# Kernel tuning notes

Hardware: AMD Instinct MI355X
Metric: run time of the kernel (lower is better)

Reference implementation:

```python
import jax, jax.numpy as jnp
import numpy as np

MARGIN = 5.0
VAR_FLOOR = 1e-4
BIG = 1e6


def setup_inputs() -> dict:
    key = jax.random.key(0)
    ks = jax.random.split(key, 8)
    B, D, R = 512, 768, 128
    C_new, C_old = 10, 100
    return {
        "features": jax.random.normal(ks[0], (B, D), jnp.float32),
        "labels": jax.random.randint(ks[1], (B,), 0, C_new),
        "new_class_ids": jnp.arange(C_new),
        "cur_means": jax.random.normal(ks[2], (C_new, D), jnp.float32),
        "cur_bases": jax.random.normal(ks[3], (C_new, D, R), jnp.float32),
        "cur_variances": jax.random.uniform(ks[4], (C_new, R + 1), jnp.float32),
        "calibrated_old_means": jax.random.normal(ks[5], (C_old, D), jnp.float32),
        "calibrated_old_bases": jax.random.normal(ks[6], (C_old, D, R), jnp.float32),
        "calibrated_old_variances": jax.random.uniform(ks[7], (C_old, R + 1), jnp.float32),
    }


def _geometry_distance_matrix(z, means, bases, variances):
    # z: [B,D], means: [C,D], bases: [C,D,R], variances: [C,R+1] -> [B,C]
    diff = z[:, None, :] - means[None, :, :]                    # [B,C,D]
    coeff = jnp.einsum('bcd,cdr->bcr', diff, bases)             # [B,C,R]
    eig = jnp.maximum(variances[:, :-1], VAR_FLOOR)             # [C,R]
    res = jnp.maximum(variances[:, -1], VAR_FLOOR)              # [C]
    parallel = jnp.sum(coeff * coeff / eig[None, :, :], axis=-1)  # [B,C]
    recon = jnp.einsum('bcr,cdr->bcd', coeff, bases)            # [B,C,D]
    residual_term = jnp.sum((diff - recon) ** 2, axis=-1) / res[None, :]
    dist = (parallel + residual_term) / z.shape[1]              # normalize_by_dim
    return jnp.nan_to_num(dist, nan=BIG, posinf=BIG, neginf=BIG)


def reference(features, labels, new_class_ids, cur_means, cur_bases, cur_variances,
              calibrated_old_means, calibrated_old_bases, calibrated_old_variances):
    z = jnp.nan_to_num(features, nan=0.0, posinf=0.0, neginf=0.0)  # [B,D]
    labels = labels.reshape(-1)

    own_all = _geometry_distance_matrix(z, cur_means, cur_bases, cur_variances)  # [B,C_new_total]
    old_all = _geometry_distance_matrix(z, calibrated_old_means, calibrated_old_bases,
                                        calibrated_old_variances)               # [B,C_old]
    old_min = jnp.min(old_all, axis=1)                                           # [B]

    # Per-new-class masks; union of class masks reproduces new_mask implicitly.
    masks = (labels[None, :] == new_class_ids[:, None]).astype(z.dtype)          # [K,B]
    counts = masks.sum(axis=1)                                                   # [K]
    denom = jnp.maximum(counts, 1.0)

    own_k = own_all[:, new_class_ids].T                                          # [K,B]
    hinge = jax.nn.relu(MARGIN + own_k - old_min[None, :])                       # [K,B]

    total_k = (hinge * masks).sum(axis=1) / denom
    own_k_mean = (own_k * masks).sum(axis=1) / denom
    old_k_mean = (old_min[None, :] * masks).sum(axis=1) / denom

    valid = (counts > 0).astype(z.dtype)
    n_valid = jnp.maximum(valid.sum(), 1.0)
    total = (total_k * valid).sum() / n_valid
    own = (own_k_mean * valid).sum() / n_valid
    old = (old_k_mean * valid).sum() / n_valid
    return jnp.stack([total, own, old])  # [total, own, old]
```

## Files before the change

### kernel.cpp

```cpp
#include <hip/hip_runtime.h>
#include <hip/hip_bf16.h>
#include <math.h>
#include <stdint.h>

#define B_N   512
#define D_N   768
#define R_N   128
#define C_NEW 10
#define C_OLD 100
#define C_TOT 110
#define MARGIN_F    5.0f
#define VAR_FLOOR_F 1e-4f
#define BIG_F       1e6f

typedef __bf16 bf16;
typedef __bf16 bf16x4 __attribute__((ext_vector_type(4)));
typedef __bf16 bf16x8 __attribute__((ext_vector_type(8)));
typedef float  f32x4  __attribute__((ext_vector_type(4)));

__device__ __forceinline__ float cleanf(float v) { return isfinite(v) ? v : 0.0f; }

__device__ __forceinline__ unsigned encf(float f) {
    unsigned u = __float_as_uint(f);
    return (u & 0x80000000u) ? ~u : (u | 0x80000000u);
}
__device__ __forceinline__ float decf(unsigned u) {
    return (u & 0x80000000u) ? __uint_as_float(u & 0x7fffffffu) : __uint_as_float(~u);
}

__global__ __launch_bounds__(256)
void prep_fused(const float* __restrict__ z,
                const float* __restrict__ cur_means, const float* __restrict__ old_means,
                const float* __restrict__ cur_bases, const float* __restrict__ old_bases,
                bf16* __restrict__ zbf, float* __restrict__ znorm, float* __restrict__ munorm,
                bf16* __restrict__ basesT, unsigned* __restrict__ ominE)
{
    const int bid = blockIdx.x;
    const int tid = threadIdx.x, wave = tid >> 6, lane = tid & 63;
    __shared__ bf16 T[128][128];
    __shared__ float s4[4];

    if (bid < 128) {
        const int b = bid * 4 + wave;
        const float4* src = (const float4*)(z + (size_t)b * D_N);
        bf16x4* dst = (bf16x4*)(zbf + (size_t)b * D_N);
        float nrm = 0.f;
        #pragma unroll
        for (int i = 0; i < 3; ++i) {
            float4 v = src[lane + i * 64];
            v.x = cleanf(v.x); v.y = cleanf(v.y); v.z = cleanf(v.z); v.w = cleanf(v.w);
            nrm += v.x * v.x + v.y * v.y + v.z * v.z + v.w * v.w;
            bf16x4 w;
            w[0] = (bf16)v.x; w[1] = (bf16)v.y; w[2] = (bf16)v.z; w[3] = (bf16)v.w;
            dst[lane + i * 64] = w;
        }
        #pragma unroll
        for (int off = 32; off >= 1; off >>= 1) nrm += __shfl_xor(nrm, off, 64);
        if (lane == 0) { znorm[b] = nrm; ominE[b] = 0xFFFFFFFFu; }
        return;
    }

    if (bid < 128 + C_TOT) {
        const int c = bid - 128;
        const float* mu = (c < C_NEW) ? cur_means + (size_t)c * D_N
                                      : old_means + (size_t)(c - C_NEW) * D_N;
        float p = 0.f;
        for (int d = tid; d < D_N; d += 256) p += mu[d] * mu[d];
        #pragma unroll
        for (int off = 32; off >= 1; off >>= 1) p += __shfl_xor(p, off, 64);
        if (lane == 0) s4[wave] = p;
        __syncthreads();
        if (tid == 0) munorm[c] = s4[0] + s4[1] + s4[2] + s4[3];
        return;
    }

    const int tb = bid - (128 + C_TOT);
    const int dt = tb % 6, c = tb / 6;
    const float* Bc = (c < C_NEW) ? cur_bases + (size_t)c * D_N * R_N
                                  : old_bases + (size_t)(c - C_NEW) * D_N * R_N;
    const int d0 = dt * 128;
    const int rg  = tid & 31;
    const int dgb = tid >> 5;

    #pragma unroll
    for (int i = 0; i < 4; ++i) {
        const int dg = i * 8 + dgb;
        const float* src = Bc + (size_t)(d0 + dg * 4) * R_N + rg * 4;
        float4 v0 = *(const float4*)(src);
        float4 v1 = *(const float4*)(src + R_N);
        float4 v2 = *(const float4*)(src + 2 * R_N);
        float4 v3 = *(const float4*)(src + 3 * R_N);
        const float* f0 = (const float*)&v0;
        const float* f1 = (const float*)&v1;
        const float* f2 = (const float*)&v2;
        const float* f3 = (const float*)&v3;
        #pragma unroll
        for (int j = 0; j < 4; ++j) {
            const int R = rg * 4 + j;
            const int pc = dg ^ (R & 31);
            bf16x4 w;
            w[0] = (bf16)f0[j]; w[1] = (bf16)f1[j]; w[2] = (bf16)f2[j]; w[3] = (bf16)f3[j];
            *(bf16x4*)(&T[R][pc * 4]) = w;
        }
    }
    __syncthreads();

    #pragma unroll
    for (int it = 0; it < 16; ++it) {
        const int q = it * 256 + tid;
        const int r = q >> 5, u = q & 31;
        const int pc = u ^ (r & 31);
        ushort4 w = *(const ushort4*)(&T[r][pc * 4]);
        *(ushort4*)(basesT + (size_t)c * R_N * D_N + (size_t)r * D_N + d0 + u * 4) = w;
    }
}

__global__ __launch_bounds__(256)
void gram(const bf16* __restrict__ basesT,
          const float* __restrict__ cur_means, const float* __restrict__ old_means,
          bf16* __restrict__ G, float* __restrict__ m_c)
{
    const int hc = blockIdx.x, c = blockIdx.y;
    const bf16* Tc = basesT + (size_t)c * R_N * D_N;
    const float* mu = (c < C_NEW) ? cur_means + (size_t)c * D_N
                                  : old_means + (size_t)(c - C_NEW) * D_N;
    __shared__ bf16 sT[128][72];
    __shared__ float sMuF[64];
    __shared__ float sRed[256];
    const int tid = threadIdx.x, wave = tid >> 6, lane = tid & 63;
    const int quad = lane >> 4, l15 = lane & 15;
    const int wr = (wave >> 1) * 64;
    const int wc = hc * 64 + (wave & 1) * 32;

    f32x4 acc[4][2];
    #pragma unroll
    for (int i = 0; i < 4; ++i)
        #pragma unroll
        for (int j = 0; j < 2; ++j) acc[i][j] = (f32x4)0.0f;
    float mAcc = 0.f;

    for (int k0 = 0; k0 < D_N; k0 += 64) {
        __syncthreads();
        #pragma unroll
        for (int p = 0; p < 4; ++p) {
            int q = p * 256 + tid, row = q >> 3, u = q & 7;
            *(uint4*)(&sT[row][u * 8]) = *(const uint4*)(Tc + (size_t)row * D_N + k0 + u * 8);
        }
        if (hc == 0 && tid < 64) sMuF[tid] = mu[k0 + tid];
        __syncthreads();
        #pragma unroll
        for (int kk = 0; kk < 64; kk += 32) {
            bf16x8 af[4], bg[2];
            #pragma unroll
            for (int i = 0; i < 4; ++i) af[i] = *(const bf16x8*)(&sT[wr + 16 * i + l15][kk + quad * 8]);
            #pragma unroll
            for (int j = 0; j < 2; ++j) bg[j] = *(const bf16x8*)(&sT[wc + 16 * j + l15][kk + quad * 8]);
            #pragma unroll
            for (int i = 0; i < 4; ++i)
                #pragma unroll
                for (int j = 0; j < 2; ++j)
                    acc[i][j] = __builtin_amdgcn_mfma_f32_16x16x32_bf16(af[i], bg[j], acc[i][j], 0, 0, 0);
        }
        if (hc == 0) {
            const int rrow = tid >> 1, hf = tid & 1;
            const bf16* tr = &sT[rrow][hf * 32];
            const float* mf = sMuF + hf * 32;
            #pragma unroll
            for (int m = 0; m < 4; ++m) {
                bf16x8 v = *(const bf16x8*)(tr + m * 8);
                #pragma unroll
                for (int e = 0; e < 8; ++e) mAcc += (float)v[e] * mf[m * 8 + e];
            }
        }
    }
    #pragma unroll
    for (int i = 0; i < 4; ++i)
        #pragma unroll
        for (int j = 0; j < 2; ++j)
            #pragma unroll
            for (int reg = 0; reg < 4; ++reg) {
                int r = wr + 16 * i + quad * 4 + reg;
                int s = wc + 16 * j + l15;
                G[(size_t)c * 16384 + (size_t)r * 128 + s] = (bf16)acc[i][j][reg];
            }
    sRed[tid] = mAcc;
    __syncthreads();
    if (hc == 0 && tid < 128) m_c[c * R_N + tid] = sRed[2 * tid] + sRed[2 * tid + 1];
}

#define PADC 136
#define SM_A   0
#define SM_B   18432
#define SM_G   0
#define SM_C   36864
#define SM_M   (36864 + 34816)
#define SM_INV (SM_M + 512)
#define SM_PAR (SM_INV + 512)
#define SM_CN  (SM_PAR + 512)
#define SM_Q   (SM_CN + 512)
#define SM_T2  (SM_Q + 512)
#define SM_MU  (SM_T2 + 3072)
#define SM_SZ  (SM_MU + 1536)

__global__ __launch_bounds__(256, 2)
void main_dist(const bf16* __restrict__ zbf, const bf16* __restrict__ basesT,
               const bf16* __restrict__ G, const float* __restrict__ m_c,
               const float* __restrict__ cur_vars, const float* __restrict__ old_vars,
               const float* __restrict__ cur_means, const float* __restrict__ old_means,
               const float* __restrict__ znorm, const float* __restrict__ munorm,
               float* __restrict__ gdist, unsigned* __restrict__ ominE)
{
    const int mt = blockIdx.x, c = blockIdx.y;
    const int b0 = mt * 128;
    const float* vars = (c < C_NEW) ? cur_vars + (size_t)c * (R_N + 1)
                                    : old_vars + (size_t)(c - C_NEW) * (R_N + 1);
    const float* mu = (c < C_NEW) ? cur_means + (size_t)c * D_N
                                  : old_means + (size_t)(c - C_NEW) * D_N;
    __shared__ __align__(16) unsigned char smem[SM_SZ];
    bf16*  sA   = (bf16*)(smem + SM_A);
    bf16*  sB   = (bf16*)(smem + SM_B);
    bf16*  sG   = (bf16*)(smem + SM_G);
    bf16*  sC   = (bf16*)(smem + SM_C);
    float* sM   = (float*)(smem + SM_M);
    float* sInv = (float*)(smem + SM_INV);
    float* sPar = (float*)(smem + SM_PAR);
    float* sCn  = (float*)(smem + SM_CN);
    float* sQ   = (float*)(smem + SM_Q);
    float* sT2  = (float*)(smem + SM_T2);
    bf16*  sMuB = (bf16*)(smem + SM_MU);

    const int tid = threadIdx.x, wave = tid >> 6, lane = tid & 63;
    const int quad = lane >> 4, l15 = lane & 15;
    const int wr = (wave >> 1) * 64, wc = (wave & 1) * 64;

    if (tid < 128) {
        sM[tid]   = m_c[c * R_N + tid];
        sInv[tid] = 1.0f / fmaxf(vars[tid], VAR_FLOOR_F);
        sQ[tid]   = 0.0f;
    }
    for (int i = tid; i < D_N; i += 256) sMuB[i] = (bf16)mu[i];

    f32x4 acc1[4][4];
    #pragma unroll
    for (int i = 0; i < 4; ++i)
        #pragma unroll
        for (int j = 0; j < 4; ++j) acc1[i][j] = (f32x4)0.0f;
    float zd = 0.f;
    const int zrow = tid >> 1, zhalf = tid & 1;

    const bf16* Az = zbf + (size_t)b0 * D_N;
    const bf16* Bb = basesT + (size_t)c * R_N * D_N;
    for (int k0 = 0; k0 < D_N; k0 += 64) {
        __syncthreads();
        #pragma unroll
        for (int p = 0; p < 4; ++p) {
            int q = p * 256 + tid, row = q >> 3, u = q & 7;
            *(uint4*)(sA + row * 72 + u * 8) = *(const uint4*)(Az + (size_t)row * D_N + k0 + u * 8);
            *(uint4*)(sB + row * 72 + u * 8) = *(const uint4*)(Bb + (size_t)row * D_N + k0 + u * 8);
        }
        __syncthreads();
        #pragma unroll
        for (int kk = 0; kk < 64; kk += 32) {
            bf16x8 af[4], bg[4];
            #pragma unroll
            for (int i = 0; i < 4; ++i) af[i] = *(const bf16x8*)(sA + (wr + 16 * i + l15) * 72 + kk + quad * 8);
            #pragma unroll
            for (int j = 0; j < 4; ++j) bg[j] = *(const bf16x8*)(sB + (wc + 16 * j + l15) * 72 + kk + quad * 8);
            #pragma unroll
            for (int i = 0; i < 4; ++i)
                #pragma unroll
                for (int j = 0; j < 4; ++j)
                    acc1[i][j] = __builtin_amdgcn_mfma_f32_16x16x32_bf16(af[i], bg[j], acc1[i][j], 0, 0, 0);
        }
        {
            const bf16* zr = sA + zrow * 72 + zhalf * 32;
            const bf16* mr = sMuB + k0 + zhalf * 32;
            #pragma unroll
            for (int m = 0; m < 4; ++m) {
                bf16x8 a = *(const bf16x8*)(zr + m * 8);
                bf16x8 b = *(const bf16x8*)(mr + m * 8);
                #pragma unroll
                for (int e = 0; e < 8; ++e) zd += (float)a[e] * (float)b[e];
            }
        }
    }
    sT2[512 + tid] = zd;

    #pragma unroll
    for (int j = 0; j < 4; ++j) {
        float mcv = sM[wc + 16 * j + l15];
        #pragma unroll
        for (int i = 0; i < 4; ++i)
            #pragma unroll
            for (int reg = 0; reg < 4; ++reg) {
                float cv = acc1[i][j][reg] - mcv;
                acc1[i][j][reg] = cv;
                int row = wr + 16 * i + quad * 4 + reg;
                int col = wc + 16 * j + l15;
                sC[row * PADC + col] = (bf16)cv;
            }
    }
    __syncthreads();

    {
        int row = tid >> 1, half = tid & 1;
        float par = 0.f, cn = 0.f;
        #pragma unroll
        for (int m = 0; m < 8; ++m) {
            bf16x8 v = *(const bf16x8*)(sC + row * PADC + half * 64 + m * 8);
            #pragma unroll
            for (int e = 0; e < 8; ++e) {
                float f = (float)v[e];
                int col = half * 64 + m * 8 + e;
                cn  += f * f;
                par += f * f * sInv[col];
            }
        }
        sT2[tid] = par;
        sT2[256 + tid] = cn;
    }
    #pragma unroll
    for (int p = 0; p < 8; ++p) {
        int q = p * 256 + tid, s = q >> 4, u = q & 15;
        *(uint4*)(sG + s * PADC + u * 8) = *(const uint4*)(G + (size_t)c * 16384 + (size_t)s * 128 + u * 8);
    }
    __syncthreads();
    if (tid < 128) {
        sPar[tid] = sT2[tid * 2] + sT2[tid * 2 + 1];
        sCn[tid]  = sT2[256 + tid * 2] + sT2[256 + tid * 2 + 1];
    }

    f32x4 acc2[4][4];
    #pragma unroll
    for (int i = 0; i < 4; ++i)
        #pragma unroll
        for (int j = 0; j < 4; ++j) acc2[i][j] = (f32x4)0.0f;
    #pragma unroll
    for (int kc = 0; kc < 128; kc += 32) {
        bf16x8 af[4], bg[4];
        #pragma unroll
        for (int i = 0; i < 4; ++i) af[i] = *(const bf16x8*)(sC + (wr + 16 * i + l15) * PADC + kc + quad * 8);
        #pragma unroll
        for (int j = 0; j < 4; ++j) bg[j] = *(const bf16x8*)(sG + (wc + 16 * j + l15) * PADC + kc + quad * 8);
        #pragma unroll
        for (int i = 0; i < 4; ++i)
            #pragma unroll
            for (int j = 0; j < 4; ++j)
                acc2[i][j] = __builtin_amdgcn_mfma_f32_16x16x32_bf16(af[i], bg[j], acc2[i][j], 0, 0, 0);
    }

    #pragma unroll
    for (int i = 0; i < 4; ++i)
        #pragma unroll
        for (int reg = 0; reg < 4; ++reg) {
            float qp = 0.f;
            #pragma unroll
            for (int j = 0; j < 4; ++j) qp += acc2[i][j][reg] * acc1[i][j][reg];
            qp += __shfl_xor(qp, 1, 64);
            qp += __shfl_xor(qp, 2, 64);
            qp += __shfl_xor(qp, 4, 64);
            qp += __shfl_xor(qp, 8, 64);
            if (l15 == 0) atomicAdd(&sQ[wr + 16 * i + quad * 4 + reg], qp);
        }
    __syncthreads();

    if (tid < 128) {
        int b = b0 + tid;
        float zdot = sT2[512 + tid * 2] + sT2[512 + tid * 2 + 1];
        float nd2 = znorm[b] - 2.0f * zdot + munorm[c];
        float res = fmaxf(vars[R_N], VAR_FLOOR_F);
        float dist = (sPar[tid] + (nd2 - 2.0f * sCn[tid] + sQ[tid]) / res) / (float)D_N;
        if (!isfinite(dist)) dist = BIG_F;
        if (c < C_NEW) {
            gdist[(size_t)b * C_NEW + c] = dist;
        } else {
            atomicMin(ominE + b, encf(dist));
        }
    }
}

__global__ __launch_bounds__(512)
void finalize(const float* __restrict__ gdist, const unsigned* __restrict__ ominE,
              const int* __restrict__ labels, const int* __restrict__ ncid,
              float* __restrict__ out)
{
    __shared__ float acc[C_NEW * 4];
    __shared__ int sNcid[C_NEW];
    const int t = threadIdx.x;
    if (t < C_NEW * 4) acc[t] = 0.f;
    if (t < C_NEW) sNcid[t] = ncid[t];
    __syncthreads();

    {
        float mn = decf(ominE[t]);
        const int lab = labels[t];
        #pragma unroll
        for (int k = 0; k < C_NEW; ++k) {
            if (lab == sNcid[k]) {
                int col = min(max(sNcid[k], 0), C_NEW - 1);
                float ow = gdist[(size_t)t * C_NEW + col];
                atomicAdd(&acc[k * 4 + 0], 1.0f);
                atomicAdd(&acc[k * 4 + 1], fmaxf(0.0f, MARGIN_F + ow - mn));
                atomicAdd(&acc[k * 4 + 2], ow);
                atomicAdd(&acc[k * 4 + 3], mn);
            }
        }
    }
    __syncthreads();

    if (t == 0) {
        float total = 0.f, own = 0.f, old = 0.f, nv = 0.f;
        #pragma unroll
        for (int k = 0; k < C_NEW; ++k) {
            float cnt = acc[k * 4 + 0];
            float den = fmaxf(cnt, 1.0f);
            if (cnt > 0.f) {
                nv += 1.f;
                total += acc[k * 4 + 1] / den;
                own   += acc[k * 4 + 2] / den;
                old   += acc[k * 4 + 3] / den;
            }
        }
        float nvd = fmaxf(nv, 1.0f);
        out[0] = total / nvd;
        out[1] = own / nvd;
        out[2] = old / nvd;
    }
}

extern "C" void kernel_launch(void* const* d_in, const int* in_sizes, int n_in,
                              void* d_out, int out_size, void* d_ws, size_t ws_size,
                              hipStream_t stream)
{
    const float* features  = (const float*)d_in[0];
    const int*   labels    = (const int*)d_in[1];
    const int*   ncid      = (const int*)d_in[2];
    const float* cur_means = (const float*)d_in[3];
    const float* cur_bases = (const float*)d_in[4];
    const float* cur_vars  = (const float*)d_in[5];
    const float* old_means = (const float*)d_in[6];
    const float* old_bases = (const float*)d_in[7];
    const float* old_vars  = (const float*)d_in[8];

    unsigned char* ws = (unsigned char*)d_ws;
    float*    gdist  = (float*)(ws + 0);
    unsigned* ominE  = (unsigned*)(ws + 20480);
    bf16*     zbf    = (bf16*) (ws + 22528);
    float*    znorm  = (float*)(ws + 808960);
    float*    munorm = (float*)(ws + 811008);
    float*    m_c    = (float*)(ws + 811520);
    bf16*     basesT = (bf16*) (ws + 867840);
    bf16*     G      = (bf16*) (ws + 22494720);

    prep_fused<<<dim3(128 + C_TOT + 6 * C_TOT), dim3(256), 0, stream>>>(
        features, cur_means, old_means, cur_bases, old_bases,
        zbf, znorm, munorm, basesT, ominE);
    gram<<<dim3(2, C_TOT), dim3(256), 0, stream>>>(basesT, cur_means, old_means, G, m_c);
    main_dist<<<dim3(4, C_TOT), dim3(256), 0, stream>>>(zbf, basesT, G, m_c,
                                                        cur_vars, old_vars,
                                                        cur_means, old_means,
                                                        znorm, munorm, gdist, ominE);
    finalize<<<dim3(1), dim3(512), 0, stream>>>(gdist, ominE, labels, ncid, (float*)d_out);
}
```

Before: 159.9 us.

## Fuse gram, distance and finalize into one kernel with last-block reduction

```diff
diff --git a/kernel.cpp b/kernel.cpp
--- a/kernel.cpp
+++ b/kernel.cpp
@@ -29,58 +29,24 @@
 }
 
 __global__ __launch_bounds__(256)
-void prep_fused(const float* __restrict__ z,
-                const float* __restrict__ cur_means, const float* __restrict__ old_means,
-                const float* __restrict__ cur_bases, const float* __restrict__ old_bases,
-                bf16* __restrict__ zbf, float* __restrict__ znorm, float* __restrict__ munorm,
-                bf16* __restrict__ basesT, unsigned* __restrict__ ominE)
+void prep_T(const float* __restrict__ cur_bases, const float* __restrict__ old_bases,
+            bf16* __restrict__ basesT, unsigned* __restrict__ ominE,
+            unsigned* __restrict__ cnt)
 {
-    const int bid = blockIdx.x;
-    const int tid = threadIdx.x, wave = tid >> 6, lane = tid & 63;
-    __shared__ bf16 T[128][128];
-    __shared__ float s4[4];
-
-    if (bid < 128) {
-        const int b = bid * 4 + wave;
-        const float4* src = (const float4*)(z + (size_t)b * D_N);
-        bf16x4* dst = (bf16x4*)(zbf + (size_t)b * D_N);
-        float nrm = 0.f;
-        #pragma unroll
-        for (int i = 0; i < 3; ++i) {
-            float4 v = src[lane + i * 64];
-            v.x = cleanf(v.x); v.y = cleanf(v.y); v.z = cleanf(v.z); v.w = cleanf(v.w);
-            nrm += v.x * v.x + v.y * v.y + v.z * v.z + v.w * v.w;
-            bf16x4 w;
-            w[0] = (bf16)v.x; w[1] = (bf16)v.y; w[2] = (bf16)v.z; w[3] = (bf16)v.w;
-            dst[lane + i * 64] = w;
-        }
-        #pragma unroll
-        for (int off = 32; off >= 1; off >>= 1) nrm += __shfl_xor(nrm, off, 64);
-        if (lane == 0) { znorm[b] = nrm; ominE[b] = 0xFFFFFFFFu; }
-        return;
-    }
-
-    if (bid < 128 + C_TOT) {
-        const int c = bid - 128;
-        const float* mu = (c < C_NEW) ? cur_means + (size_t)c * D_N
-                                      : old_means + (size_t)(c - C_NEW) * D_N;
-        float p = 0.f;
-        for (int d = tid; d < D_N; d += 256) p += mu[d] * mu[d];
-        #pragma unroll
-        for (int off = 32; off >= 1; off >>= 1) p += __shfl_xor(p, off, 64);
-        if (lane == 0) s4[wave] = p;
-        __syncthreads();
-        if (tid == 0) munorm[c] = s4[0] + s4[1] + s4[2] + s4[3];
-        return;
-    }
-
-    const int tb = bid - (128 + C_TOT);
-    const int dt = tb % 6, c = tb / 6;
+    const int bid = blockIdx.x, t = threadIdx.x;
+    if (bid == 0) {
+        ominE[t] = 0xFFFFFFFFu;
+        ominE[256 + t] = 0xFFFFFFFFu;
+        if (t == 0) *cnt = 0u;
+    }
+
+    const int dt = bid % 6, c = bid / 6;
     const float* Bc = (c < C_NEW) ? cur_bases + (size_t)c * D_N * R_N
                                   : old_bases + (size_t)(c - C_NEW) * D_N * R_N;
+    __shared__ bf16 T[128][128];
     const int d0 = dt * 128;
-    const int rg  = tid & 31;
-    const int dgb = tid >> 5;
+    const int rg  = t & 31;
+    const int dgb = t >> 5;
 
     #pragma unroll
     for (int i = 0; i < 4; ++i) {
@@ -107,7 +73,7 @@
 
     #pragma unroll
     for (int it = 0; it < 16; ++it) {
-        const int q = it * 256 + tid;
+        const int q = it * 256 + t;
         const int r = q >> 5, u = q & 31;
         const int pc = u ^ (r & 31);
         ushort4 w = *(const ushort4*)(&T[r][pc * 4]);
@@ -115,316 +81,265 @@
     }
 }
 
-__global__ __launch_bounds__(256)
-void gram(const bf16* __restrict__ basesT,
-          const float* __restrict__ cur_means, const float* __restrict__ old_means,
-          bf16* __restrict__ G, float* __restrict__ m_c)
-{
-    const int hc = blockIdx.x, c = blockIdx.y;
-    const bf16* Tc = basesT + (size_t)c * R_N * D_N;
-    const float* mu = (c < C_NEW) ? cur_means + (size_t)c * D_N
-                                  : old_means + (size_t)(c - C_NEW) * D_N;
-    __shared__ bf16 sT[128][72];
-    __shared__ float sMuF[64];
-    __shared__ float sRed[256];
-    const int tid = threadIdx.x, wave = tid >> 6, lane = tid & 63;
-    const int quad = lane >> 4, l15 = lane & 15;
-    const int wr = (wave >> 1) * 64;
-    const int wc = hc * 64 + (wave & 1) * 32;
-
-    f32x4 acc[4][2];
-    #pragma unroll
-    for (int i = 0; i < 4; ++i)
-        #pragma unroll
-        for (int j = 0; j < 2; ++j) acc[i][j] = (f32x4)0.0f;
-    float mAcc = 0.f;
-
-    for (int k0 = 0; k0 < D_N; k0 += 64) {
-        __syncthreads();
-        #pragma unroll
-        for (int p = 0; p < 4; ++p) {
-            int q = p * 256 + tid, row = q >> 3, u = q & 7;
-            *(uint4*)(&sT[row][u * 8]) = *(const uint4*)(Tc + (size_t)row * D_N + k0 + u * 8);
-        }
-        if (hc == 0 && tid < 64) sMuF[tid] = mu[k0 + tid];
-        __syncthreads();
-        #pragma unroll
-        for (int kk = 0; kk < 64; kk += 32) {
-            bf16x8 af[4], bg[2];
-            #pragma unroll
-            for (int i = 0; i < 4; ++i) af[i] = *(const bf16x8*)(&sT[wr + 16 * i + l15][kk + quad * 8]);
-            #pragma unroll
-            for (int j = 0; j < 2; ++j) bg[j] = *(const bf16x8*)(&sT[wc + 16 * j + l15][kk + quad * 8]);
-            #pragma unroll
-            for (int i = 0; i < 4; ++i)
-                #pragma unroll
-                for (int j = 0; j < 2; ++j)
-                    acc[i][j] = __builtin_amdgcn_mfma_f32_16x16x32_bf16(af[i], bg[j], acc[i][j], 0, 0, 0);
-        }
-        if (hc == 0) {
-            const int rrow = tid >> 1, hf = tid & 1;
-            const bf16* tr = &sT[rrow][hf * 32];
-            const float* mf = sMuF + hf * 32;
-            #pragma unroll
-            for (int m = 0; m < 4; ++m) {
-                bf16x8 v = *(const bf16x8*)(tr + m * 8);
-                #pragma unroll
-                for (int e = 0; e < 8; ++e) mAcc += (float)v[e] * mf[m * 8 + e];
-            }
-        }
-    }
-    #pragma unroll
-    for (int i = 0; i < 4; ++i)
-        #pragma unroll
-        for (int j = 0; j < 2; ++j)
-            #pragma unroll
-            for (int reg = 0; reg < 4; ++reg) {
-                int r = wr + 16 * i + quad * 4 + reg;
-                int s = wc + 16 * j + l15;
-                G[(size_t)c * 16384 + (size_t)r * 128 + s] = (bf16)acc[i][j][reg];
-            }
-    sRed[tid] = mAcc;
-    __syncthreads();
-    if (hc == 0 && tid < 128) m_c[c * R_N + tid] = sRed[2 * tid] + sRed[2 * tid + 1];
-}
-
 #define PADC 136
 #define SM_A   0
 #define SM_B   18432
-#define SM_G   0
-#define SM_C   36864
-#define SM_M   (36864 + 34816)
-#define SM_INV (SM_M + 512)
-#define SM_PAR (SM_INV + 512)
-#define SM_CN  (SM_PAR + 512)
-#define SM_Q   (SM_CN + 512)
-#define SM_T2  (SM_Q + 512)
-#define SM_MU  (SM_T2 + 3072)
-#define SM_SZ  (SM_MU + 1536)
+#define SM_C   0
+#define SM_G   36864
+#define SM_MU  71680
+#define SM_INV 74752
+#define SM_Q   75264
+#define SM_PAR 75776
+#define SM_CN  76288
+#define SM_ND  76800
+#define SM_T2  77312
+#define SM_FL  79360
+#define SM_SZ  79376
 
 __global__ __launch_bounds__(256, 2)
-void main_dist(const bf16* __restrict__ zbf, const bf16* __restrict__ basesT,
-               const bf16* __restrict__ G, const float* __restrict__ m_c,
-               const float* __restrict__ cur_vars, const float* __restrict__ old_vars,
-               const float* __restrict__ cur_means, const float* __restrict__ old_means,
-               const float* __restrict__ znorm, const float* __restrict__ munorm,
-               float* __restrict__ gdist, unsigned* __restrict__ ominE)
+void main_all(const float* __restrict__ z, const bf16* __restrict__ basesT,
+              const float* __restrict__ cur_vars, const float* __restrict__ old_vars,
+              const float* __restrict__ cur_means, const float* __restrict__ old_means,
+              const int* __restrict__ labels, const int* __restrict__ ncid,
+              float* __restrict__ gdist, unsigned* __restrict__ ominE,
+              unsigned* __restrict__ cnt, float* __restrict__ out)
 {
-    const int mt = blockIdx.x, c = blockIdx.y;
-    const int b0 = mt * 128;
-    const float* vars = (c < C_NEW) ? cur_vars + (size_t)c * (R_N + 1)
-                                    : old_vars + (size_t)(c - C_NEW) * (R_N + 1);
-    const float* mu = (c < C_NEW) ? cur_means + (size_t)c * D_N
-                                  : old_means + (size_t)(c - C_NEW) * D_N;
     __shared__ __align__(16) unsigned char smem[SM_SZ];
     bf16*  sA   = (bf16*)(smem + SM_A);
     bf16*  sB   = (bf16*)(smem + SM_B);
+    bf16*  sC   = (bf16*)(smem + SM_C);
     bf16*  sG   = (bf16*)(smem + SM_G);
-    bf16*  sC   = (bf16*)(smem + SM_C);
-    float* sM   = (float*)(smem + SM_M);
+    float* sMu  = (float*)(smem + SM_MU);
     float* sInv = (float*)(smem + SM_INV);
+    float* sQ   = (float*)(smem + SM_Q);
     float* sPar = (float*)(smem + SM_PAR);
     float* sCn  = (float*)(smem + SM_CN);
-    float* sQ   = (float*)(smem + SM_Q);
+    float* sNd  = (float*)(smem + SM_ND);
     float* sT2  = (float*)(smem + SM_T2);
-    bf16*  sMuB = (bf16*)(smem + SM_MU);
+    unsigned* sFl = (unsigned*)(smem + SM_FL);
 
     const int tid = threadIdx.x, wave = tid >> 6, lane = tid & 63;
     const int quad = lane >> 4, l15 = lane & 15;
     const int wr = (wave >> 1) * 64, wc = (wave & 1) * 64;
 
-    if (tid < 128) {
-        sM[tid]   = m_c[c * R_N + tid];
-        sInv[tid] = 1.0f / fmaxf(vars[tid], VAR_FLOOR_F);
-        sQ[tid]   = 0.0f;
-    }
-    for (int i = tid; i < D_N; i += 256) sMuB[i] = (bf16)mu[i];
-
-    f32x4 acc1[4][4];
-    #pragma unroll
-    for (int i = 0; i < 4; ++i)
-        #pragma unroll
-        for (int j = 0; j < 4; ++j) acc1[i][j] = (f32x4)0.0f;
-    float zd = 0.f;
-    const int zrow = tid >> 1, zhalf = tid & 1;
-
-    const bf16* Az = zbf + (size_t)b0 * D_N;
-    const bf16* Bb = basesT + (size_t)c * R_N * D_N;
-    for (int k0 = 0; k0 < D_N; k0 += 64) {
-        __syncthreads();
-        #pragma unroll
-        for (int p = 0; p < 4; ++p) {
-            int q = p * 256 + tid, row = q >> 3, u = q & 7;
-            *(uint4*)(sA + row * 72 + u * 8) = *(const uint4*)(Az + (size_t)row * D_N + k0 + u * 8);
-            *(uint4*)(sB + row * 72 + u * 8) = *(const uint4*)(Bb + (size_t)row * D_N + k0 + u * 8);
-        }
-        __syncthreads();
-        #pragma unroll
-        for (int kk = 0; kk < 64; kk += 32) {
+    const int fid = blockIdx.x;
+    const int c  = (fid & 7) + 8 * (fid >> 5);
+    const int mt = (fid >> 3) & 3;
+
+    if (c < C_TOT) {
+        const int b0 = mt * 128;
+        const float* vars = (c < C_NEW) ? cur_vars + (size_t)c * (R_N + 1)
+                                        : old_vars + (size_t)(c - C_NEW) * (R_N + 1);
+        const float* mu = (c < C_NEW) ? cur_means + (size_t)c * D_N
+                                      : old_means + (size_t)(c - C_NEW) * D_N;
+
+        if (tid < 128) {
+            sInv[tid] = 1.0f / fmaxf(vars[tid], VAR_FLOOR_F);
+            sQ[tid] = 0.0f;
+        }
+        for (int i = tid; i < D_N; i += 256) sMu[i] = mu[i];
+
+        f32x4 acc1[4][4], accG[4][4];
+        #pragma unroll
+        for (int i = 0; i < 4; ++i)
+            #pragma unroll
+            for (int j = 0; j < 4; ++j) { acc1[i][j] = (f32x4)0.0f; accG[i][j] = (f32x4)0.0f; }
+        float nd2p[8];
+        #pragma unroll
+        for (int p = 0; p < 8; ++p) nd2p[p] = 0.f;
+
+        const int rb = tid >> 4, f4 = tid & 15;
+        const float* Az = z + (size_t)b0 * D_N;
+        const bf16*  Bb = basesT + (size_t)c * R_N * D_N;
+
+        for (int k0 = 0; k0 < D_N; k0 += 64) {
+            __syncthreads();
+            #pragma unroll
+            for (int p = 0; p < 4; ++p) {
+                int q = p * 256 + tid, row = q >> 3, u = q & 7;
+                *(uint4*)(sB + row * 72 + u * 8) = *(const uint4*)(Bb + (size_t)row * D_N + k0 + u * 8);
+            }
+            {
+                float4 m4 = *(const float4*)(sMu + k0 + f4 * 4);
+                #pragma unroll
+                for (int p = 0; p < 8; ++p) {
+                    int row = p * 16 + rb;
+                    float4 v = *(const float4*)(Az + (size_t)row * D_N + k0 + f4 * 4);
+                    float d0 = cleanf(v.x) - m4.x;
+                    float d1 = cleanf(v.y) - m4.y;
+                    float d2 = cleanf(v.z) - m4.z;
+                    float d3 = cleanf(v.w) - m4.w;
+                    nd2p[p] += d0 * d0 + d1 * d1 + d2 * d2 + d3 * d3;
+                    bf16x4 w;
+                    w[0] = (bf16)d0; w[1] = (bf16)d1; w[2] = (bf16)d2; w[3] = (bf16)d3;
+                    *(bf16x4*)(sA + row * 72 + f4 * 4) = w;
+                }
+            }
+            __syncthreads();
+            #pragma unroll
+            for (int kk = 0; kk < 64; kk += 32) {
+                bf16x8 afA[4], bgB[4], afB[4];
+                #pragma unroll
+                for (int i = 0; i < 4; ++i) afA[i] = *(const bf16x8*)(sA + (wr + 16 * i + l15) * 72 + kk + quad * 8);
+                #pragma unroll
+                for (int j = 0; j < 4; ++j) bgB[j] = *(const bf16x8*)(sB + (wc + 16 * j + l15) * 72 + kk + quad * 8);
+                #pragma unroll
+                for (int i = 0; i < 4; ++i) afB[i] = *(const bf16x8*)(sB + (wr + 16 * i + l15) * 72 + kk + quad * 8);
+                #pragma unroll
+                for (int i = 0; i < 4; ++i)
+                    #pragma unroll
+                    for (int j = 0; j < 4; ++j) {
+                        acc1[i][j] = __builtin_amdgcn_mfma_f32_16x16x32_bf16(afA[i], bgB[j], acc1[i][j], 0, 0, 0);
+                        accG[i][j] = __builtin_amdgcn_mfma_f32_16x16x32_bf16(afB[i], bgB[j], accG[i][j], 0, 0, 0);
+                    }
+            }
+        }
+
+        #pragma unroll
+        for (int p = 0; p < 8; ++p) {
+            float s = nd2p[p];
+            s += __shfl_xor(s, 1, 64); s += __shfl_xor(s, 2, 64);
+            s += __shfl_xor(s, 4, 64); s += __shfl_xor(s, 8, 64);
+            if (l15 == 0) sNd[p * 16 + rb] = s;
+        }
+
+        #pragma unroll
+        for (int i = 0; i < 4; ++i)
+            #pragma unroll
+            for (int j = 0; j < 4; ++j)
+                #pragma unroll
+                for (int reg = 0; reg < 4; ++reg)
+                    sG[(wr + 16 * i + quad * 4 + reg) * PADC + wc + 16 * j + l15] = (bf16)accG[i][j][reg];
+        __syncthreads();
+
+        #pragma unroll
+        for (int i = 0; i < 4; ++i)
+            #pragma unroll
+            for (int j = 0; j < 4; ++j)
+                #pragma unroll
+                for (int reg = 0; reg < 4; ++reg)
+                    sC[(wr + 16 * i + quad * 4 + reg) * PADC + wc + 16 * j + l15] = (bf16)acc1[i][j][reg];
+        __syncthreads();
+
+        {
+            int row = tid >> 1, half = tid & 1;
+            float par = 0.f, cn = 0.f;
+            #pragma unroll
+            for (int m = 0; m < 8; ++m) {
+                bf16x8 v = *(const bf16x8*)(sC + row * PADC + half * 64 + m * 8);
+                #pragma unroll
+                for (int e = 0; e < 8; ++e) {
+                    float f = (float)v[e];
+                    int col = half * 64 + m * 8 + e;
+                    cn  += f * f;
+                    par += f * f * sInv[col];
+                }
+            }
+            sT2[tid] = par;
+            sT2[256 + tid] = cn;
+        }
+        __syncthreads();
+        if (tid < 128) {
+            sPar[tid] = sT2[tid * 2] + sT2[tid * 2 + 1];
+            sCn[tid]  = sT2[256 + tid * 2] + sT2[256 + tid * 2 + 1];
+        }
+
+        f32x4 acc2[4][4];
+        #pragma unroll
+        for (int i = 0; i < 4; ++i)
+            #pragma unroll
+            for (int j = 0; j < 4; ++j) acc2[i][j] = (f32x4)0.0f;
+        #pragma unroll
+        for (int kc = 0; kc < 128; kc += 32) {
             bf16x8 af[4], bg[4];
             #pragma unroll
-            for (int i = 0; i < 4; ++i) af[i] = *(const bf16x8*)(sA + (wr + 16 * i + l15) * 72 + kk + quad * 8);
-            #pragma unroll
-            for (int j = 0; j < 4; ++j) bg[j] = *(const bf16x8*)(sB + (wc + 16 * j + l15) * 72 + kk + quad * 8);
+            for (int i = 0; i < 4; ++i) af[i] = *(const bf16x8*)(sC + (wr + 16 * i + l15) * PADC + kc + quad * 8);
+            #pragma unroll
+            for (int j = 0; j < 4; ++j) bg[j] = *(const bf16x8*)(sG + (wc + 16 * j + l15) * PADC + kc + quad * 8);
             #pragma unroll
             for (int i = 0; i < 4; ++i)
                 #pragma unroll
                 for (int j = 0; j < 4; ++j)
-                    acc1[i][j] = __builtin_amdgcn_mfma_f32_16x16x32_bf16(af[i], bg[j], acc1[i][j], 0, 0, 0);
-        }
-        {
-            const bf16* zr = sA + zrow * 72 + zhalf * 32;
-            const bf16* mr = sMuB + k0 + zhalf * 32;
-            #pragma unroll
-            for (int m = 0; m < 4; ++m) {
-                bf16x8 a = *(const bf16x8*)(zr + m * 8);
-                bf16x8 b = *(const bf16x8*)(mr + m * 8);
-                #pragma unroll
-                for (int e = 0; e < 8; ++e) zd += (float)a[e] * (float)b[e];
-            }
-        }
-    }
-    sT2[512 + tid] = zd;
-
-    #pragma unroll
-    for (int j = 0; j < 4; ++j) {
-        float mcv = sM[wc + 16 * j + l15];
+                    acc2[i][j] = __builtin_amdgcn_mfma_f32_16x16x32_bf16(af[i], bg[j], acc2[i][j], 0, 0, 0);
+        }
+
         #pragma unroll
         for (int i = 0; i < 4; ++i)
             #pragma unroll
             for (int reg = 0; reg < 4; ++reg) {
-                float cv = acc1[i][j][reg] - mcv;
-                acc1[i][j][reg] = cv;
-                int row = wr + 16 * i + quad * 4 + reg;
-                int col = wc + 16 * j + l15;
-                sC[row * PADC + col] = (bf16)cv;
-            }
-    }
+                float qp = 0.f;
+                #pragma unroll
+                for (int j = 0; j < 4; ++j) qp += acc2[i][j][reg] * acc1[i][j][reg];
+                qp += __shfl_xor(qp, 1, 64);
+                qp += __shfl_xor(qp, 2, 64);
+                qp += __shfl_xor(qp, 4, 64);
+                qp += __shfl_xor(qp, 8, 64);
+                if (l15 == 0) atomicAdd(&sQ[wr + 16 * i + quad * 4 + reg], qp);
+            }
+        __syncthreads();
+
+        if (tid < 128) {
+            int b = b0 + tid;
+            float res = fmaxf(vars[R_N], VAR_FLOOR_F);
+            float dist = (sPar[tid] + (sNd[tid] - 2.0f * sCn[tid] + sQ[tid]) / res) / (float)D_N;
+            if (!isfinite(dist)) dist = BIG_F;
+            if (c < C_NEW) {
+                gdist[(size_t)b * C_NEW + c] = dist;
+            } else {
+                atomicMin(ominE + b, encf(dist));
+            }
+        }
+    }
+
     __syncthreads();
-
-    {
-        int row = tid >> 1, half = tid & 1;
-        float par = 0.f, cn = 0.f;
-        #pragma unroll
-        for (int m = 0; m < 8; ++m) {
-            bf16x8 v = *(const bf16x8*)(sC + row * PADC + half * 64 + m * 8);
-            #pragma unroll
-            for (int e = 0; e < 8; ++e) {
-                float f = (float)v[e];
-                int col = half * 64 + m * 8 + e;
-                cn  += f * f;
-                par += f * f * sInv[col];
-            }
-        }
-        sT2[tid] = par;
-        sT2[256 + tid] = cn;
-    }
-    #pragma unroll
-    for (int p = 0; p < 8; ++p) {
-        int q = p * 256 + tid, s = q >> 4, u = q & 15;
-        *(uint4*)(sG + s * PADC + u * 8) = *(const uint4*)(G + (size_t)c * 16384 + (size_t)s * 128 + u * 8);
+    if (tid == 0) {
+        __threadfence();
+        sFl[0] = atomicAdd(cnt, 1u);
     }
     __syncthreads();
-    if (tid < 128) {
-        sPar[tid] = sT2[tid * 2] + sT2[tid * 2 + 1];
-        sCn[tid]  = sT2[256 + tid * 2] + sT2[256 + tid * 2 + 1];
-    }
-
-    f32x4 acc2[4][4];
-    #pragma unroll
-    for (int i = 0; i < 4; ++i)
-        #pragma unroll
-        for (int j = 0; j < 4; ++j) acc2[i][j] = (f32x4)0.0f;
-    #pragma unroll
-    for (int kc = 0; kc < 128; kc += 32) {
-        bf16x8 af[4], bg[4];
-        #pragma unroll
-        for (int i = 0; i < 4; ++i) af[i] = *(const bf16x8*)(sC + (wr + 16 * i + l15) * PADC + kc + quad * 8);
-        #pragma unroll
-        for (int j = 0; j < 4; ++j) bg[j] = *(const bf16x8*)(sG + (wc + 16 * j + l15) * PADC + kc + quad * 8);
-        #pragma unroll
-        for (int i = 0; i < 4; ++i)
-            #pragma unroll
-            for (int j = 0; j < 4; ++j)
-                acc2[i][j] = __builtin_amdgcn_mfma_f32_16x16x32_bf16(af[i], bg[j], acc2[i][j], 0, 0, 0);
-    }
-
-    #pragma unroll
-    for (int i = 0; i < 4; ++i)
-        #pragma unroll
-        for (int reg = 0; reg < 4; ++reg) {
-            float qp = 0.f;
-            #pragma unroll
-            for (int j = 0; j < 4; ++j) qp += acc2[i][j][reg] * acc1[i][j][reg];
-            qp += __shfl_xor(qp, 1, 64);
-            qp += __shfl_xor(qp, 2, 64);
-            qp += __shfl_xor(qp, 4, 64);
-            qp += __shfl_xor(qp, 8, 64);
-            if (l15 == 0) atomicAdd(&sQ[wr + 16 * i + quad * 4 + reg], qp);
-        }
-    __syncthreads();
-
-    if (tid < 128) {
-        int b = b0 + tid;
-        float zdot = sT2[512 + tid * 2] + sT2[512 + tid * 2 + 1];
-        float nd2 = znorm[b] - 2.0f * zdot + munorm[c];
-        float res = fmaxf(vars[R_N], VAR_FLOOR_F);
-        float dist = (sPar[tid] + (nd2 - 2.0f * sCn[tid] + sQ[tid]) / res) / (float)D_N;
-        if (!isfinite(dist)) dist = BIG_F;
-        if (c < C_NEW) {
-            gdist[(size_t)b * C_NEW + c] = dist;
-        } else {
-            atomicMin(ominE + b, encf(dist));
-        }
-    }
-}
-
-__global__ __launch_bounds__(512)
-void finalize(const float* __restrict__ gdist, const unsigned* __restrict__ ominE,
-              const int* __restrict__ labels, const int* __restrict__ ncid,
-              float* __restrict__ out)
-{
-    __shared__ float acc[C_NEW * 4];
-    __shared__ int sNcid[C_NEW];
-    const int t = threadIdx.x;
-    if (t < C_NEW * 4) acc[t] = 0.f;
-    if (t < C_NEW) sNcid[t] = ncid[t];
-    __syncthreads();
-
-    {
-        float mn = decf(ominE[t]);
-        const int lab = labels[t];
-        #pragma unroll
-        for (int k = 0; k < C_NEW; ++k) {
-            if (lab == sNcid[k]) {
-                int col = min(max(sNcid[k], 0), C_NEW - 1);
-                float ow = gdist[(size_t)t * C_NEW + col];
-                atomicAdd(&acc[k * 4 + 0], 1.0f);
-                atomicAdd(&acc[k * 4 + 1], fmaxf(0.0f, MARGIN_F + ow - mn));
-                atomicAdd(&acc[k * 4 + 2], ow);
-                atomicAdd(&acc[k * 4 + 3], mn);
-            }
-        }
-    }
-    __syncthreads();
-
-    if (t == 0) {
-        float total = 0.f, own = 0.f, old = 0.f, nv = 0.f;
-        #pragma unroll
-        for (int k = 0; k < C_NEW; ++k) {
-            float cnt = acc[k * 4 + 0];
-            float den = fmaxf(cnt, 1.0f);
-            if (cnt > 0.f) {
-                nv += 1.f;
-                total += acc[k * 4 + 1] / den;
-                own   += acc[k * 4 + 2] / den;
-                old   += acc[k * 4 + 3] / den;
-            }
-        }
-        float nvd = fmaxf(nv, 1.0f);
-        out[0] = total / nvd;
-        out[1] = own / nvd;
-        out[2] = old / nvd;
+    if (sFl[0] == 447u) {
+        __threadfence();
+        float* accF = sT2;
+        int* ncidS = (int*)(sT2 + 48);
+        if (tid < 40) accF[tid] = 0.f;
+        if (tid < C_NEW) ncidS[tid] = ncid[tid];
+        __syncthreads();
+        #pragma unroll
+        for (int rep = 0; rep < 2; ++rep) {
+            int b = rep * 256 + tid;
+            float mn = decf(ominE[b]);
+            int lab = labels[b];
+            #pragma unroll
+            for (int k = 0; k < C_NEW; ++k) {
+                if (lab == ncidS[k]) {
+                    int col = min(max(ncidS[k], 0), C_NEW - 1);
+                    float ow = gdist[(size_t)b * C_NEW + col];
+                    atomicAdd(&accF[k * 4 + 0], 1.0f);
+                    atomicAdd(&accF[k * 4 + 1], fmaxf(0.0f, MARGIN_F + ow - mn));
+                    atomicAdd(&accF[k * 4 + 2], ow);
+                    atomicAdd(&accF[k * 4 + 3], mn);
+                }
+            }
+        }
+        __syncthreads();
+        if (tid == 0) {
+            float total = 0.f, own = 0.f, old = 0.f, nv = 0.f;
+            #pragma unroll
+            for (int k = 0; k < C_NEW; ++k) {
+                float cntk = accF[k * 4 + 0];
+                float den = fmaxf(cntk, 1.0f);
+                if (cntk > 0.f) {
+                    nv += 1.f;
+                    total += accF[k * 4 + 1] / den;
+                    own   += accF[k * 4 + 2] / den;
+                    old   += accF[k * 4 + 3] / den;
+                }
+            }
+            float nvd = fmaxf(nv, 1.0f);
+            out[0] = total / nvd;
+            out[1] = own / nvd;
+            out[2] = old / nvd;
+        }
     }
 }
 
@@ -445,20 +360,14 @@
     unsigned char* ws = (unsigned char*)d_ws;
     float*    gdist  = (float*)(ws + 0);
     unsigned* ominE  = (unsigned*)(ws + 20480);
-    bf16*     zbf    = (bf16*) (ws + 22528);
-    float*    znorm  = (float*)(ws + 808960);
-    float*    munorm = (float*)(ws + 811008);
-    float*    m_c    = (float*)(ws + 811520);
-    bf16*     basesT = (bf16*) (ws + 867840);
-    bf16*     G      = (bf16*) (ws + 22494720);
-
-    prep_fused<<<dim3(128 + C_TOT + 6 * C_TOT), dim3(256), 0, stream>>>(
-        features, cur_means, old_means, cur_bases, old_bases,
-        zbf, znorm, munorm, basesT, ominE);
-    gram<<<dim3(2, C_TOT), dim3(256), 0, stream>>>(basesT, cur_means, old_means, G, m_c);
-    main_dist<<<dim3(4, C_TOT), dim3(256), 0, stream>>>(zbf, basesT, G, m_c,
-                                                        cur_vars, old_vars,
-                                                        cur_means, old_means,
-                                                        znorm, munorm, gdist, ominE);
-    finalize<<<dim3(1), dim3(512), 0, stream>>>(gdist, ominE, labels, ncid, (float*)d_out);
-}
+    unsigned* cnt    = (unsigned*)(ws + 22528);
+    bf16*     basesT = (bf16*) (ws + 22544);
+
+    prep_T<<<dim3(6 * C_TOT), dim3(256), 0, stream>>>(cur_bases, old_bases,
+                                                      basesT, ominE, cnt);
+    main_all<<<dim3(448), dim3(256), 0, stream>>>(features, basesT,
+                                                  cur_vars, old_vars,
+                                                  cur_means, old_means,
+                                                  labels, ncid,
+                                                  gdist, ominE, cnt, (float*)d_out);
+}
```

New measurement: 165.5 us. +3.5%, slower.
